# Kernel tuning notes

Hardware: AMD Instinct MI355X
Metric: run time of the kernel (lower is better)

Reference implementation:

```python
import jax, jax.numpy as jnp
import numpy as np

# ---- model hyperparameters (match init_kwargs) ----
THRESHOLD = 1.0
DECAY = 0.9
RESET = 0.0
BATCH = 256
INPUT_DIM = 1024
HIDDEN_DIM = 2048
OUTPUT_DIM = 10
NUM_LAYERS = 2
SIM_STEPS = 100
SPIKE_PROB = 0.2  # density of input spike bins


def setup_inputs() -> dict:
    key = jax.random.key(0)
    k1, k2, k3, k4 = jax.random.split(key, 4)
    # binary spike bins: [B, input_dim, T]
    input_bins = (jax.random.uniform(k1, (BATCH, INPUT_DIM, SIM_STEPS)) < SPIKE_PROB).astype(jnp.float32)
    W_ih = jax.random.normal(k2, (INPUT_DIM, HIDDEN_DIM), dtype=jnp.float32) * 0.1
    W_hh = jax.random.normal(k3, (NUM_LAYERS - 1, HIDDEN_DIM, HIDDEN_DIM), dtype=jnp.float32) * 0.1
    W_ho = jax.random.normal(k4, (HIDDEN_DIM, OUTPUT_DIM), dtype=jnp.float32) * 0.1
    return {"input_bins": input_bins, "W_ih": W_ih, "W_hh": W_hh, "W_ho": W_ho}


def _lif_step(v, current):
    """One leaky-integrate-and-fire update. v, current: [B, N]."""
    v = v * DECAY + current
    spiked = v >= THRESHOLD
    spikes = jnp.where(spiked, 1.0, 0.0).astype(v.dtype)
    v = jnp.where(spiked, RESET, v)
    return v, spikes


def reference(input_bins, W_ih, W_hh, W_ho):
    B = input_bins.shape[0]
    T = input_bins.shape[2]
    x = jnp.transpose(input_bins, (2, 0, 1))  # [T, B, input_dim]
    v_hidden = tuple(jnp.zeros((B, W_ih.shape[1]), input_bins.dtype) for _ in range(NUM_LAYERS))
    v_out = jnp.zeros((B, W_ho.shape[1]), input_bins.dtype)

    def step(carry, inp_t):
        vs, vo = carry
        vs = list(vs)
        vs[0], s = _lif_step(vs[0], inp_t @ W_ih)
        for i in range(NUM_LAYERS - 1):
            vs[i + 1], s = _lif_step(vs[i + 1], s @ W_hh[i])
        # modulator signal is 0 here -> output_input * (1 + 0*0.1) = output_input
        vo, s_out = _lif_step(vo, s @ W_ho)
        return (tuple(vs), vo), s_out

    _, out_spikes = jax.lax.scan(step, (v_hidden, v_out), x)  # [T, B, output_dim]
    output_rates = out_spikes.sum(axis=0) / T  # [B, output_dim]
    return output_rates
```

## Files before the change

### kernel.cpp

```cpp
#include <hip/hip_runtime.h>
#include <hip/hip_bf16.h>


#define B 256
#define IN_DIM 1024
#define HID 2048
#define OUT_DIM 10
#define T_STEPS 100
#define NCH 4
#define RT (T_STEPS * B)

typedef unsigned long long ull;
typedef int v4i __attribute__((ext_vector_type(4)));

template<int K>
__global__ __launch_bounds__(256) void cvt_w_i8(
    const float* __restrict__ W, signed char* __restrict__ Bq)
{
    constexpr int WPR = K / 64;
    size_t id = (size_t)blockIdx.x * 256 + threadIdx.x;
    if (id >= (size_t)(K / 4) * HID) return;
    int n  = (int)(id % HID);
    int kg = (int)(id / HID);
    int k0 = kg * 4;
    signed char dig[4][4];
#pragma unroll
    for (int i = 0; i < 4; ++i) {
        double w = (double)W[(size_t)(k0 + i) * HID + n];
        long long V = __double2ll_rn(w * 2147483648.0);
#pragma unroll
        for (int c = 0; c < 3; ++c) {
            int r = (int)(signed char)(V & 0xFF);
            dig[c][i] = (signed char)r;
            V = (V - r) >> 8;
        }
        dig[3][i] = (signed char)V;
    }
    int wb = k0 >> 6, lk = (k0 >> 4) & 3, jj = k0 & 15;
    int nb32 = n >> 5, ct = (n >> 4) & 1, li = n & 15;
    int lane = lk * 16 + li;
    size_t base = ((size_t)nb32 * WPR + wb) * 8192 + (size_t)lane * 16 + jj;
#pragma unroll
    for (int c = 0; c < 4; ++c) {
        int pc = c * 2 + ct;
        unsigned pk = (unsigned)(unsigned char)dig[c][0]
                    | ((unsigned)(unsigned char)dig[c][1] << 8)
                    | ((unsigned)(unsigned char)dig[c][2] << 16)
                    | ((unsigned)(unsigned char)dig[c][3] << 24);
        *reinterpret_cast<unsigned*>(Bq + base + (size_t)pc * 1024) = pk;
    }
}

__global__ __launch_bounds__(256) void cvt_who_i8(
    const float* __restrict__ who, signed char* __restrict__ Bq3)
{
    int id = blockIdx.x * 256 + threadIdx.x;
    if (id >= 32 * 64 * 4) return;
    int jg = id & 3;
    int lane = (id >> 2) & 63;
    int w = id >> 8;
    int li = lane & 15, lk = lane >> 4;
    signed char dig[4][4];
#pragma unroll
    for (int i = 0; i < 4; ++i) {
        int jj = jg * 4 + i;
        int k = w * 64 + lk * 16 + jj;
        double x = (li < OUT_DIM) ? (double)who[(size_t)k * OUT_DIM + li] : 0.0;
        long long V = __double2ll_rn(x * 2147483648.0);
#pragma unroll
        for (int c = 0; c < 3; ++c) {
            int r = (int)(signed char)(V & 0xFF);
            dig[c][i] = (signed char)r;
            V = (V - r) >> 8;
        }
        dig[3][i] = (signed char)V;
    }
    size_t base = (size_t)w * 4096 + (size_t)lane * 16 + jg * 4;
#pragma unroll
    for (int c = 0; c < 4; ++c) {
        unsigned pk = (unsigned)(unsigned char)dig[c][0]
                    | ((unsigned)(unsigned char)dig[c][1] << 8)
                    | ((unsigned)(unsigned char)dig[c][2] << 16)
                    | ((unsigned)(unsigned char)dig[c][3] << 24);
        *reinterpret_cast<unsigned*>(Bq3 + base + (size_t)c * 1024) = pk;
    }
}

__global__ __launch_bounds__(256) void bitpack_input(
    const float* __restrict__ inp, ull* __restrict__ XbitsT)
{
    __shared__ float sb[4][64][33];
    const int wv = threadIdx.x >> 6;
    const int lane = threadIdx.x & 63;
    const int g = blockIdx.x * 4 + wv;
    const int b = g >> 4;
    const int ig = g & 15;
    const float* __restrict__ src = inp + ((size_t)b * IN_DIM + ig * 64) * T_STEPS;
    ull* __restrict__ dst = XbitsT + (size_t)ig * RT + b;

#pragma unroll
    for (int tc = 0; tc < 4; ++tc) {
        const int t0 = tc * 32;
        if (tc < 3) {
#pragma unroll
            for (int f4 = 0; f4 < 32; ++f4) {
                int f = f4 * 64 + lane;
                int ii = f >> 5, tt = f & 31;
                sb[wv][ii][tt] = src[ii * T_STEPS + t0 + tt];
            }
        } else {
#pragma unroll
            for (int f4 = 0; f4 < 4; ++f4) {
                int f = f4 * 64 + lane;
                int ii = f >> 2, tt = f & 3;
                sb[wv][ii][tt] = src[ii * T_STEPS + t0 + tt];
            }
        }
        __syncthreads();
        const int len = (tc < 3) ? 32 : 4;
        for (int tt = 0; tt < len; ++tt) {
            float v = sb[wv][lane][tt];
            ull m = __ballot(v > 0.5f);
            if (lane == 0) dst[(size_t)(t0 + tt) * B] = m;
        }
        __syncthreads();
    }
}

template<int K>
__global__ __launch_bounds__(256, 3) void gemm_i8(
    const ull* __restrict__ bitsT, int row_base,
    const signed char* __restrict__ Bq, float* __restrict__ C)
{
    constexpr int WPR = K / 64;
    constexpr int NP  = WPR / 2;
    __shared__ __align__(16) signed char blds[6][8192];

    const int tid = threadIdx.x;
    const int lane = tid & 63;
    const int wv = __builtin_amdgcn_readfirstlane(tid >> 6);
    const int row0 = blockIdx.x * 128;
    const int c0 = blockIdx.y * 32;
    const int li = lane & 15;
    const int lk = lane >> 4;
    const int sh = lk * 16;
    const int r0l = wv * 32;

    const signed char* __restrict__ bsrc = Bq + (size_t)blockIdx.y * WPR * 8192;
    const ull* __restrict__ m0p = bitsT + (row_base + row0 + r0l + li);
    const ull* __restrict__ m1p = m0p + 16;

    auto stage_b = [&](int w, int slot) {
        const signed char* src = bsrc + (size_t)w * 8192 + lane * 16;
        signed char* db = &blds[0][0] + slot * 8192;
        __builtin_amdgcn_global_load_lds(
            (const __attribute__((address_space(1))) unsigned int*)(src + wv * 1024),
            (__attribute__((address_space(3))) unsigned int*)(db + wv * 1024), 16, 0, 0);
        __builtin_amdgcn_global_load_lds(
            (const __attribute__((address_space(1))) unsigned int*)(src + (wv + 4) * 1024),
            (__attribute__((address_space(3))) unsigned int*)(db + (wv + 4) * 1024), 16, 0, 0);
    };

    stage_b(0, 0);
    stage_b(1, 1);
    stage_b(2, 2);
    stage_b(3, 3);
    ull r0[4], r1[4];
#pragma unroll
    for (int u = 0; u < 4; ++u) {
        r0[u] = m0p[(size_t)u * RT];
        r1[u] = m1p[(size_t)u * RT];
    }
    __syncthreads();

    v4i acc[2][2][NCH];
#pragma unroll
    for (int g = 0; g < 2; ++g)
#pragma unroll
        for (int t = 0; t < 2; ++t)
#pragma unroll
            for (int c = 0; c < NCH; ++c) acc[g][t][c] = (v4i){0, 0, 0, 0};

    int s0 = 0;
#pragma unroll 1
    for (int p2 = 0; p2 < NP; p2 += 2) {
#pragma unroll
        for (int pp = 0; pp < 2; ++pp) {
            const int w0 = (p2 + pp) * 2;
            const int u0 = w0 & 3, u1 = (w0 + 1) & 3;
            int s1 = s0 + 1; if (s1 >= 6) s1 -= 6;
            int t0 = s0 + 4; if (t0 >= 6) t0 -= 6;
            int t1 = s0 + 5; if (t1 >= 6) t1 -= 6;

            int wn0 = w0 + 4; if (wn0 >= WPR) wn0 -= WPR;
            int wn1 = w0 + 5; if (wn1 >= WPR) wn1 -= WPR;
            stage_b(wn0, t0);
            stage_b(wn1, t1);
            ull m00 = r0[u0], m01 = r1[u0];
            ull m10 = r0[u1], m11 = r1[u1];
            r0[u0] = m0p[(size_t)wn0 * RT];
            r1[u0] = m1p[(size_t)wn0 * RT];
            r0[u1] = m0p[(size_t)wn1 * RT];
            r1[u1] = m1p[(size_t)wn1 * RT];

            {
                unsigned sa = (unsigned)(m00 >> sh) & 0xFFFFu;
                unsigned sb = (unsigned)(m01 >> sh) & 0xFFFFu;
                v4i a0, a1;
#pragma unroll
                for (int d = 0; d < 4; ++d) {
                    a0[d] = (int)((((sa >> (4 * d)) & 0xFu) * 0x00204081u) & 0x01010101u);
                    a1[d] = (int)((((sb >> (4 * d)) & 0xFu) * 0x00204081u) & 0x01010101u);
                }
                const signed char* bb = &blds[0][0] + s0 * 8192 + lane * 16;
                __builtin_amdgcn_s_setprio(1);
#pragma unroll
                for (int c = 0; c < NCH; ++c) {
#pragma unroll
                    for (int t = 0; t < 2; ++t) {
                        v4i b = *(const v4i*)(bb + (c * 2 + t) * 1024);
                        acc[0][t][c] = __builtin_amdgcn_mfma_i32_16x16x64_i8(a0, b, acc[0][t][c], 0, 0, 0);
                        acc[1][t][c] = __builtin_amdgcn_mfma_i32_16x16x64_i8(a1, b, acc[1][t][c], 0, 0, 0);
                    }
                }
                __builtin_amdgcn_s_setprio(0);
            }
            {
                unsigned sa = (unsigned)(m10 >> sh) & 0xFFFFu;
                unsigned sb = (unsigned)(m11 >> sh) & 0xFFFFu;
                v4i a0, a1;
#pragma unroll
                for (int d = 0; d < 4; ++d) {
                    a0[d] = (int)((((sa >> (4 * d)) & 0xFu) * 0x00204081u) & 0x01010101u);
                    a1[d] = (int)((((sb >> (4 * d)) & 0xFu) * 0x00204081u) & 0x01010101u);
                }
                const signed char* bb = &blds[0][0] + s1 * 8192 + lane * 16;
                __builtin_amdgcn_s_setprio(1);
#pragma unroll
                for (int c = 0; c < NCH; ++c) {
#pragma unroll
                    for (int t = 0; t < 2; ++t) {
                        v4i b = *(const v4i*)(bb + (c * 2 + t) * 1024);
                        acc[0][t][c] = __builtin_amdgcn_mfma_i32_16x16x64_i8(a0, b, acc[0][t][c], 0, 0, 0);
                        acc[1][t][c] = __builtin_amdgcn_mfma_i32_16x16x64_i8(a1, b, acc[1][t][c], 0, 0, 0);
                    }
                }
                __builtin_amdgcn_s_setprio(0);
            }

            __asm__ __volatile__("s_waitcnt vmcnt(12)\n\ts_barrier" ::: "memory");
            s0 += 2; if (s0 >= 6) s0 -= 6;
        }
    }

#pragma unroll
    for (int g = 0; g < 2; ++g) {
#pragma unroll
        for (int t = 0; t < 2; ++t) {
#pragma unroll
            for (int r = 0; r < 4; ++r) {
                long long V = (long long)acc[g][t][3][r];
                V = (V << 8) + (long long)acc[g][t][2][r];
                V = (V << 8) + (long long)acc[g][t][1][r];
                V = (V << 8) + (long long)acc[g][t][0][r];
                C[(size_t)(row0 + r0l + g * 16 + lk * 4 + r) * HID + c0 + t * 16 + li] =
                    (float)((double)V * 0x1p-31);
            }
        }
    }
}

__global__ __launch_bounds__(256) void gemm_out(
    const ull* __restrict__ bitsT, int row_base,
    const signed char* __restrict__ Bq3, double* __restrict__ C3)
{
    const int lane = threadIdx.x & 63;
    const int wv = threadIdx.x >> 6;
    const int li = lane & 15;
    const int lk = lane >> 4;
    const int sh = lk * 16;
    const int row0 = blockIdx.x * 256 + wv * 64;
    const ull* __restrict__ mp = bitsT + (row_base + row0 + li);

    v4i acc[4][NCH];
#pragma unroll
    for (int g = 0; g < 4; ++g)
#pragma unroll
        for (int c = 0; c < NCH; ++c) acc[g][c] = (v4i){0, 0, 0, 0};

#pragma unroll 1
    for (int w = 0; w < 32; ++w) {
        ull m[4];
#pragma unroll
        for (int g = 0; g < 4; ++g) m[g] = mp[(size_t)w * RT + g * 16];
        const v4i* __restrict__ bp = (const v4i*)(Bq3 + (size_t)w * 4096 + (size_t)lane * 16);
        v4i b[NCH];
#pragma unroll
        for (int c = 0; c < NCH; ++c) b[c] = bp[c * 64];
#pragma unroll
        for (int g = 0; g < 4; ++g) {
            unsigned s = (unsigned)(m[g] >> sh) & 0xFFFFu;
            v4i a;
#pragma unroll
            for (int d = 0; d < 4; ++d)
                a[d] = (int)((((s >> (4 * d)) & 0xFu) * 0x00204081u) & 0x01010101u);
#pragma unroll
            for (int c = 0; c < NCH; ++c)
                acc[g][c] = __builtin_amdgcn_mfma_i32_16x16x64_i8(a, b[c], acc[g][c], 0, 0, 0);
        }
    }

    if (li < OUT_DIM) {
#pragma unroll
        for (int g = 0; g < 4; ++g) {
#pragma unroll
            for (int rr = 0; rr < 4; ++rr) {
                long long V = (long long)acc[g][3][rr];
                V = (V << 8) + (long long)acc[g][2][rr];
                V = (V << 8) + (long long)acc[g][1][rr];
                V = (V << 8) + (long long)acc[g][0][rr];
                C3[(size_t)(row0 + g * 16 + lk * 4 + rr) * OUT_DIM + li] =
                    (double)V * 0x1p-31;
            }
        }
    }
}

__global__ __launch_bounds__(256) void lif_scan(
    const float* __restrict__ C, double* __restrict__ vstate,
    ull* __restrict__ SbitsT, int row_base, int Tl, int first)
{
    int g = blockIdx.x * 4 + (threadIdx.x >> 6);
    int lane = threadIdx.x & 63;
    int b = g >> 5;
    int ng = g & 31;
    int n = ng * 64 + lane;
    const float* __restrict__ Cp = C + (size_t)b * HID + n;
    ull* __restrict__ Sp = SbitsT + (size_t)ng * RT + row_base + b;
    double v = first ? 0.0 : vstate[(size_t)b * HID + n];
    int tl = 0;
    for (; tl + 4 <= Tl; tl += 4) {
        float c0 = Cp[(size_t)(tl + 0) * (B * HID)];
        float c1 = Cp[(size_t)(tl + 1) * (B * HID)];
        float c2 = Cp[(size_t)(tl + 2) * (B * HID)];
        float c3 = Cp[(size_t)(tl + 3) * (B * HID)];
#pragma unroll
        for (int i = 0; i < 4; ++i) {
            float cc = (i == 0) ? c0 : (i == 1) ? c1 : (i == 2) ? c2 : c3;
            v = v * 0.9 + (double)cc;
            bool s = (v >= 1.0);
            if (s) v = 0.0;
            ull mask = __ballot(s);
            if (lane == 0) Sp[(size_t)(tl + i) * B] = mask;
        }
    }
    for (; tl < Tl; ++tl) {
        double c = (double)Cp[(size_t)tl * (B * HID)];
        v = v * 0.9 + c;
        bool s = (v >= 1.0);
        if (s) v = 0.0;
        ull mask = __ballot(s);
        if (lane == 0) Sp[(size_t)tl * B] = mask;
    }
    vstate[(size_t)b * HID + n] = v;
}

__global__ __launch_bounds__(256) void lif_out(
    const double* __restrict__ C3, double* __restrict__ vstate,
    int* __restrict__ cnt_state, float* __restrict__ out, int Tl, int first)
{
    int tid = blockIdx.x * 256 + threadIdx.x;
    if (tid >= B * OUT_DIM) return;
    int b = tid / OUT_DIM, o = tid % OUT_DIM;
    const double* __restrict__ Cp = C3 + (size_t)b * OUT_DIM + o;
    double v = first ? 0.0 : vstate[tid];
    int cnt = first ? 0 : cnt_state[tid];
    int tl = 0;
    for (; tl + 4 <= Tl; tl += 4) {
        double c0 = Cp[(size_t)(tl + 0) * (B * OUT_DIM)];
        double c1 = Cp[(size_t)(tl + 1) * (B * OUT_DIM)];
        double c2 = Cp[(size_t)(tl + 2) * (B * OUT_DIM)];
        double c3 = Cp[(size_t)(tl + 3) * (B * OUT_DIM)];
#pragma unroll
        for (int i = 0; i < 4; ++i) {
            double cc = (i == 0) ? c0 : (i == 1) ? c1 : (i == 2) ? c2 : c3;
            v = v * 0.9 + cc;
            if (v >= 1.0) { cnt++; v = 0.0; }
        }
    }
    for (; tl < Tl; ++tl) {
        double c = Cp[(size_t)tl * (B * OUT_DIM)];
        v = v * 0.9 + c;
        if (v >= 1.0) { cnt++; v = 0.0; }
    }
    vstate[tid] = v;
    cnt_state[tid] = cnt;
    out[tid] = (float)((double)cnt / (double)T_STEPS);
}

extern "C" void kernel_launch(void* const* d_in, const int* in_sizes, int n_in,
                              void* d_out, int out_size, void* d_ws, size_t ws_size,
                              hipStream_t stream) {
    const float* inp = (const float*)d_in[0];
    const float* wih = (const float*)d_in[1];
    const float* whh = (const float*)d_in[2];
    const float* who = (const float*)d_in[3];
    float* out = (float*)d_out;

    unsigned char* p = (unsigned char*)d_ws;
    auto alloc = [&](size_t sz) -> void* {
        void* r = (void*)p;
        p += (sz + 255) & ~(size_t)255;
        return r;
    };
    signed char* Bq1 = (signed char*)alloc((size_t)NCH * HID * IN_DIM + 4096);
    signed char* Bq2 = (signed char*)alloc((size_t)NCH * HID * HID + 4096);
    signed char* Bq3 = (signed char*)alloc((size_t)32 * 4096 + 4096);
    ull* XbitsT = (ull*)alloc((size_t)16 * RT * 8);
    ull* S1T    = (ull*)alloc((size_t)32 * RT * 8);
    ull* S2T    = (ull*)alloc((size_t)32 * RT * 8);
    double* v1 = (double*)alloc((size_t)B * HID * 8);
    double* v2 = (double*)alloc((size_t)B * HID * 8);
    double* vo = (double*)alloc((size_t)B * OUT_DIM * 8);
    int* cnts  = (int*)alloc((size_t)B * OUT_DIM * 4);

    size_t used = (size_t)(p - (unsigned char*)d_ws);
    size_t remain = (ws_size > used) ? (ws_size - used) : 0;
    size_t per_t = (size_t)B * HID * 4 + (size_t)B * OUT_DIM * 8 + 1024;
    int CH = (int)(remain / per_t);
    if (CH > T_STEPS) CH = T_STEPS;
    if (CH < 1) CH = 1;
    double* C3 = (double*)alloc((size_t)CH * B * OUT_DIM * 8);
    float* C   = (float*)alloc((size_t)CH * B * HID * 4);

    cvt_w_i8<IN_DIM><<<((IN_DIM / 4) * HID + 255) / 256, 256, 0, stream>>>(wih, Bq1);
    cvt_w_i8<HID><<<((HID / 4) * HID + 255) / 256, 256, 0, stream>>>(whh, Bq2);
    cvt_who_i8<<<32, 256, 0, stream>>>(who, Bq3);
    bitpack_input<<<(B * (IN_DIM / 64)) / 4, 256, 0, stream>>>(inp, XbitsT);

    for (int t0 = 0; t0 < T_STEPS; t0 += CH) {
        int L = T_STEPS - t0;
        if (L > CH) L = CH;
        int rows = L * B;
        int first = (t0 == 0) ? 1 : 0;

        gemm_i8<IN_DIM><<<dim3(rows / 128, HID / 32), 256, 0, stream>>>(
            XbitsT, t0 * B, Bq1, C);
        lif_scan<<<(B * (HID / 64)) / 4, 256, 0, stream>>>(
            C, v1, S1T, t0 * B, L, first);

        gemm_i8<HID><<<dim3(rows / 128, HID / 32), 256, 0, stream>>>(
            S1T, t0 * B, Bq2, C);
        lif_scan<<<(B * (HID / 64)) / 4, 256, 0, stream>>>(
            C, v2, S2T, t0 * B, L, first);

        gemm_out<<<rows / 256, 256, 0, stream>>>(S2T, t0 * B, Bq3, C3);
        lif_out<<<(B * OUT_DIM + 255) / 256, 256, 0, stream>>>(
            C3, vo, cnts, out, L, first);
    }
}
```

Measured before the change: 859.1 us.

## Switch int8 spike GEMM to 32x32x32 MFMA with matching weight layout

```diff
diff --git a/kernel.cpp b/kernel.cpp
--- a/kernel.cpp
+++ b/kernel.cpp
@@ -12,6 +12,7 @@
 
 typedef unsigned long long ull;
 typedef int v4i __attribute__((ext_vector_type(4)));
+typedef int v16i __attribute__((ext_vector_type(16)));
 
 template<int K>
 __global__ __launch_bounds__(256) void cvt_w_i8(
@@ -21,8 +22,8 @@
     size_t id = (size_t)blockIdx.x * 256 + threadIdx.x;
     if (id >= (size_t)(K / 4) * HID) return;
     int n  = (int)(id % HID);
-    int kg = (int)(id / HID);
-    int k0 = kg * 4;
+    int kg4 = (int)(id / HID);
+    int k0 = kg4 * 4;
     signed char dig[4][4];
 #pragma unroll
     for (int i = 0; i < 4; ++i) {
@@ -36,13 +37,13 @@
         }
         dig[3][i] = (signed char)V;
     }
-    int wb = k0 >> 6, lk = (k0 >> 4) & 3, jj = k0 & 15;
-    int nb32 = n >> 5, ct = (n >> 4) & 1, li = n & 15;
-    int lane = lk * 16 + li;
+    int wb = k0 >> 6, khalf = (k0 >> 5) & 1, kg = (k0 >> 4) & 1, jj = k0 & 15;
+    int nb32 = n >> 5, col = n & 31;
+    int lane = kg * 32 + col;
     size_t base = ((size_t)nb32 * WPR + wb) * 8192 + (size_t)lane * 16 + jj;
 #pragma unroll
     for (int c = 0; c < 4; ++c) {
-        int pc = c * 2 + ct;
+        int pc = (c < 3) ? (c * 2 + khalf) : (6 + khalf);
         unsigned pk = (unsigned)(unsigned char)dig[c][0]
                     | ((unsigned)(unsigned char)dig[c][1] << 8)
                     | ((unsigned)(unsigned char)dig[c][2] << 16)
@@ -133,7 +134,7 @@
     const signed char* __restrict__ Bq, float* __restrict__ C)
 {
     constexpr int WPR = K / 64;
-    constexpr int NP  = WPR / 2;
+    constexpr int NW  = WPR / 2;
     __shared__ __align__(16) signed char blds[6][8192];
 
     const int tid = threadIdx.x;
@@ -141,14 +142,13 @@
     const int wv = __builtin_amdgcn_readfirstlane(tid >> 6);
     const int row0 = blockIdx.x * 128;
     const int c0 = blockIdx.y * 32;
-    const int li = lane & 15;
-    const int lk = lane >> 4;
-    const int sh = lk * 16;
+    const int col = lane & 31;
+    const int kg  = lane >> 5;
+    const int kgsh = kg * 16;
     const int r0l = wv * 32;
 
     const signed char* __restrict__ bsrc = Bq + (size_t)blockIdx.y * WPR * 8192;
-    const ull* __restrict__ m0p = bitsT + (row_base + row0 + r0l + li);
-    const ull* __restrict__ m1p = m0p + 16;
+    const ull* __restrict__ mp = bitsT + (row_base + row0 + r0l + col);
 
     auto stage_b = [&](int w, int slot) {
         const signed char* src = bsrc + (size_t)w * 8192 + lane * 16;
@@ -165,29 +165,33 @@
     stage_b(1, 1);
     stage_b(2, 2);
     stage_b(3, 3);
-    ull r0[4], r1[4];
-#pragma unroll
-    for (int u = 0; u < 4; ++u) {
-        r0[u] = m0p[(size_t)u * RT];
-        r1[u] = m1p[(size_t)u * RT];
-    }
+    ull r[4];
+#pragma unroll
+    for (int u = 0; u < 4; ++u) r[u] = mp[(size_t)u * RT];
     __syncthreads();
 
-    v4i acc[2][2][NCH];
-#pragma unroll
-    for (int g = 0; g < 2; ++g)
-#pragma unroll
-        for (int t = 0; t < 2; ++t)
-#pragma unroll
-            for (int c = 0; c < NCH; ++c) acc[g][t][c] = (v4i){0, 0, 0, 0};
+    v16i acc[NCH];
+#pragma unroll
+    for (int c = 0; c < NCH; ++c)
+#pragma unroll
+        for (int q = 0; q < 16; ++q) acc[c][q] = 0;
+
+    auto expand = [&](unsigned x) -> v4i {
+        v4i a;
+#pragma unroll
+        for (int d = 0; d < 4; ++d)
+            a[d] = (int)((((x >> (4 * d)) & 0xFu) * 0x00204081u) & 0x01010101u);
+        return a;
+    };
 
     int s0 = 0;
 #pragma unroll 1
-    for (int p2 = 0; p2 < NP; p2 += 2) {
+    for (int p2 = 0; p2 < NW; p2 += 2) {
 #pragma unroll
         for (int pp = 0; pp < 2; ++pp) {
             const int w0 = (p2 + pp) * 2;
-            const int u0 = w0 & 3, u1 = (w0 + 1) & 3;
+            const int u0 = (2 * pp) & 3;
+            const int u1 = u0 + 1;
             int s1 = s0 + 1; if (s1 >= 6) s1 -= 6;
             int t0 = s0 + 4; if (t0 >= 6) t0 -= 6;
             int t1 = s0 + 5; if (t1 >= 6) t1 -= 6;
@@ -196,77 +200,59 @@
             int wn1 = w0 + 5; if (wn1 >= WPR) wn1 -= WPR;
             stage_b(wn0, t0);
             stage_b(wn1, t1);
-            ull m00 = r0[u0], m01 = r1[u0];
-            ull m10 = r0[u1], m11 = r1[u1];
-            r0[u0] = m0p[(size_t)wn0 * RT];
-            r1[u0] = m1p[(size_t)wn0 * RT];
-            r0[u1] = m0p[(size_t)wn1 * RT];
-            r1[u1] = m1p[(size_t)wn1 * RT];
+            ull m0 = r[u0], m1 = r[u1];
+            r[u0] = mp[(size_t)wn0 * RT];
+            r[u1] = mp[(size_t)wn1 * RT];
 
             {
-                unsigned sa = (unsigned)(m00 >> sh) & 0xFFFFu;
-                unsigned sb = (unsigned)(m01 >> sh) & 0xFFFFu;
-                v4i a0, a1;
-#pragma unroll
-                for (int d = 0; d < 4; ++d) {
-                    a0[d] = (int)((((sa >> (4 * d)) & 0xFu) * 0x00204081u) & 0x01010101u);
-                    a1[d] = (int)((((sb >> (4 * d)) & 0xFu) * 0x00204081u) & 0x01010101u);
+                const signed char* bb = &blds[0][0] + s0 * 8192 + lane * 16;
+                v4i a0 = expand((unsigned)(m0 >> kgsh) & 0xFFFFu);
+                v4i a1 = expand((unsigned)(m0 >> (32 + kgsh)) & 0xFFFFu);
+                __builtin_amdgcn_s_setprio(1);
+#pragma unroll
+                for (int c = 0; c < NCH; ++c) {
+                    v4i b0 = *(const v4i*)(bb + ((c < 3 ? c * 2 : 6) + 0) * 1024);
+                    acc[c] = __builtin_amdgcn_mfma_i32_32x32x32_i8(a0, b0, acc[c], 0, 0, 0);
                 }
-                const signed char* bb = &blds[0][0] + s0 * 8192 + lane * 16;
-                __builtin_amdgcn_s_setprio(1);
 #pragma unroll
                 for (int c = 0; c < NCH; ++c) {
-#pragma unroll
-                    for (int t = 0; t < 2; ++t) {
-                        v4i b = *(const v4i*)(bb + (c * 2 + t) * 1024);
-                        acc[0][t][c] = __builtin_amdgcn_mfma_i32_16x16x64_i8(a0, b, acc[0][t][c], 0, 0, 0);
-                        acc[1][t][c] = __builtin_amdgcn_mfma_i32_16x16x64_i8(a1, b, acc[1][t][c], 0, 0, 0);
-                    }
+                    v4i b1 = *(const v4i*)(bb + ((c < 3 ? c * 2 : 6) + 1) * 1024);
+                    acc[c] = __builtin_amdgcn_mfma_i32_32x32x32_i8(a1, b1, acc[c], 0, 0, 0);
                 }
                 __builtin_amdgcn_s_setprio(0);
             }
             {
-                unsigned sa = (unsigned)(m10 >> sh) & 0xFFFFu;
-                unsigned sb = (unsigned)(m11 >> sh) & 0xFFFFu;
-                v4i a0, a1;
-#pragma unroll
-                for (int d = 0; d < 4; ++d) {
-                    a0[d] = (int)((((sa >> (4 * d)) & 0xFu) * 0x00204081u) & 0x01010101u);
-                    a1[d] = (int)((((sb >> (4 * d)) & 0xFu) * 0x00204081u) & 0x01010101u);
+                const signed char* bb = &blds[0][0] + s1 * 8192 + lane * 16;
+                v4i a0 = expand((unsigned)(m1 >> kgsh) & 0xFFFFu);
+                v4i a1 = expand((unsigned)(m1 >> (32 + kgsh)) & 0xFFFFu);
+                __builtin_amdgcn_s_setprio(1);
+#pragma unroll
+                for (int c = 0; c < NCH; ++c) {
+                    v4i b0 = *(const v4i*)(bb + ((c < 3 ? c * 2 : 6) + 0) * 1024);
+                    acc[c] = __builtin_amdgcn_mfma_i32_32x32x32_i8(a0, b0, acc[c], 0, 0, 0);
                 }
-                const signed char* bb = &blds[0][0] + s1 * 8192 + lane * 16;
-                __builtin_amdgcn_s_setprio(1);
 #pragma unroll
                 for (int c = 0; c < NCH; ++c) {
-#pragma unroll
-                    for (int t = 0; t < 2; ++t) {
-                        v4i b = *(const v4i*)(bb + (c * 2 + t) * 1024);
-                        acc[0][t][c] = __builtin_amdgcn_mfma_i32_16x16x64_i8(a0, b, acc[0][t][c], 0, 0, 0);
-                        acc[1][t][c] = __builtin_amdgcn_mfma_i32_16x16x64_i8(a1, b, acc[1][t][c], 0, 0, 0);
-                    }
+                    v4i b1 = *(const v4i*)(bb + ((c < 3 ? c * 2 : 6) + 1) * 1024);
+                    acc[c] = __builtin_amdgcn_mfma_i32_32x32x32_i8(a1, b1, acc[c], 0, 0, 0);
                 }
                 __builtin_amdgcn_s_setprio(0);
             }
 
-            __asm__ __volatile__("s_waitcnt vmcnt(12)\n\ts_barrier" ::: "memory");
+            __asm__ __volatile__("s_waitcnt vmcnt(8)\n\ts_barrier" ::: "memory");
             s0 += 2; if (s0 >= 6) s0 -= 6;
         }
     }
 
 #pragma unroll
-    for (int g = 0; g < 2; ++g) {
-#pragma unroll
-        for (int t = 0; t < 2; ++t) {
-#pragma unroll
-            for (int r = 0; r < 4; ++r) {
-                long long V = (long long)acc[g][t][3][r];
-                V = (V << 8) + (long long)acc[g][t][2][r];
-                V = (V << 8) + (long long)acc[g][t][1][r];
-                V = (V << 8) + (long long)acc[g][t][0][r];
-                C[(size_t)(row0 + r0l + g * 16 + lk * 4 + r) * HID + c0 + t * 16 + li] =
-                    (float)((double)V * 0x1p-31);
-            }
-        }
+    for (int rr = 0; rr < 16; ++rr) {
+        long long V = (long long)acc[3][rr];
+        V = (V << 8) + (long long)acc[2][rr];
+        V = (V << 8) + (long long)acc[1][rr];
+        V = (V << 8) + (long long)acc[0][rr];
+        int rloc = (rr & 3) + 8 * (rr >> 2) + 4 * kg;
+        C[(size_t)(row0 + r0l + rloc) * HID + c0 + col] =
+            (float)((double)V * 0x1p-31);
     }
 }
 
@@ -339,15 +325,14 @@
     ull* __restrict__ Sp = SbitsT + (size_t)ng * RT + row_base + b;
     double v = first ? 0.0 : vstate[(size_t)b * HID + n];
     int tl = 0;
-    for (; tl + 4 <= Tl; tl += 4) {
-        float c0 = Cp[(size_t)(tl + 0) * (B * HID)];
-        float c1 = Cp[(size_t)(tl + 1) * (B * HID)];
-        float c2 = Cp[(size_t)(tl + 2) * (B * HID)];
-        float c3 = Cp[(size_t)(tl + 3) * (B * HID)];
-#pragma unroll
-        for (int i = 0; i < 4; ++i) {
-            float cc = (i == 0) ? c0 : (i == 1) ? c1 : (i == 2) ? c2 : c3;
-            v = v * 0.9 + (double)cc;
+    for (; tl + 8 <= Tl; tl += 8) {
+        float cc[8];
+#pragma unroll
+        for (int i = 0; i < 8; ++i)
+            cc[i] = Cp[(size_t)(tl + i) * (B * HID)];
+#pragma unroll
+        for (int i = 0; i < 8; ++i) {
+            v = v * 0.9 + (double)cc[i];
             bool s = (v >= 1.0);
             if (s) v = 0.0;
             ull mask = __ballot(s);
```

Result: slower. 938.1 us (+9.2%).
